# Optimization experiments

Measured on AMD Instinct MI355X. Metric: run time of the kernel, lower is better.

The kernel has to match this reference:

```python
import jax, jax.numpy as jnp
import numpy as np


def _kabsch_rmsd(p, c):
    # p, c: [N, 3]
    pm = jnp.mean(p, axis=0)  # [3]
    cm = jnp.mean(c, axis=0)  # [3]
    # 3x3 cross-covariance
    A = (p - pm).T @ (c - cm)
    U, S, Vt = jnp.linalg.svd(A, full_matrices=False)
    d = jnp.sign(jnp.linalg.det(A))
    # corr_mat = diag([1, 1, d]);  rotation = U @ corr_mat @ Vt
    scale = jnp.concatenate([jnp.ones((2,), dtype=p.dtype), d[None].astype(p.dtype)])
    R = U @ (scale[:, None] * Vt)  # [3,3]
    # translation = pm - R @ cm; aligned coords = (R @ c^T)^T + translation
    aligned = c @ R.T + (pm - R @ cm)
    sq = jnp.sum((p - aligned) ** 2, axis=1)  # [N]
    return jnp.sqrt(jnp.mean(sq))


def setup_inputs() -> dict:
    key = jax.random.key(0)
    k1, k2 = jax.random.split(key)
    B, N = 4096, 2048
    coords_pred = jax.random.normal(k1, (B, N, 3), dtype=jnp.float32)
    coords = jax.random.normal(k2, (B, N, 3), dtype=jnp.float32)
    return {"coords_pred": coords_pred, "coords": coords}


def reference(coords_pred, coords):
    # Batched Kabsch alignment + RMSD; default mode='global', return_all=False
    # -> mean over the per-sample RMSDs.
    rmsds = jax.vmap(_kabsch_rmsd)(coords_pred, coords)  # [B]
    return jnp.mean(rmsds)
```

## Files before the change

### kernel.cpp

```cpp
#include <hip/hip_runtime.h>
#include <math.h>

#define NPTS 2048
#define BLOCK 256

__global__ __launch_bounds__(BLOCK) void kabsch_kernel(
    const float* __restrict__ P, const float* __restrict__ C,
    float* __restrict__ out, int B) {
  const int b = blockIdx.x;
  const int t = threadIdx.x;
  const float4* p4 = (const float4*)(P + (size_t)b * (NPTS * 3));
  const float4* c4 = (const float4*)(C + (size_t)b * (NPTS * 3));

  float acc[17];
#pragma unroll
  for (int i = 0; i < 17; i++) acc[i] = 0.f;

#pragma unroll
  for (int k = 0; k < (NPTS * 3 / 4) / (BLOCK * 3); k++) {
    const int base = k * (BLOCK * 3) + 3 * t;
    const float4 pa = p4[base], pb = p4[base + 1], pq = p4[base + 2];
    const float4 ca = c4[base], cb = c4[base + 1], cq = c4[base + 2];
    const float Px[4] = {pa.x, pa.w, pb.z, pq.y};
    const float Py[4] = {pa.y, pb.x, pb.w, pq.z};
    const float Pz[4] = {pa.z, pb.y, pq.x, pq.w};
    const float Cx[4] = {ca.x, ca.w, cb.z, cq.y};
    const float Cy[4] = {ca.y, cb.x, cb.w, cq.z};
    const float Cz[4] = {ca.z, cb.y, cq.x, cq.w};
#pragma unroll
    for (int i = 0; i < 4; i++) {
      const float px = Px[i], py = Py[i], pz = Pz[i];
      const float cx = Cx[i], cy = Cy[i], cz = Cz[i];
      acc[0] += px; acc[1] += py; acc[2] += pz;
      acc[3] += cx; acc[4] += cy; acc[5] += cz;
      acc[6] += px * px + py * py + pz * pz;
      acc[7] += cx * cx + cy * cy + cz * cz;
      acc[8]  += px * cx; acc[9]  += px * cy; acc[10] += px * cz;
      acc[11] += py * cx; acc[12] += py * cy; acc[13] += py * cz;
      acc[14] += pz * cx; acc[15] += pz * cy; acc[16] += pz * cz;
    }
  }

#pragma unroll
  for (int off = 32; off > 0; off >>= 1) {
#pragma unroll
    for (int i = 0; i < 17; i++) acc[i] += __shfl_down(acc[i], off);
  }
  __shared__ float red[BLOCK / 64][17];
  const int wave = t >> 6, lane = t & 63;
  if (lane == 0) {
#pragma unroll
    for (int i = 0; i < 17; i++) red[wave][i] = acc[i];
  }
  __syncthreads();

  if (t == 0) {
    double s[17];
#pragma unroll
    for (int i = 0; i < 17; i++) {
      float v = red[0][i];
      for (int w = 1; w < BLOCK / 64; w++) v += red[w][i];
      s[i] = (double)v;
    }
    const double invN = 1.0 / (double)NPTS;
    const double spx = s[0], spy = s[1], spz = s[2];
    const double scx = s[3], scy = s[4], scz = s[5];
    const double Ep = s[6] - (spx * spx + spy * spy + spz * spz) * invN;
    const double Ec = s[7] - (scx * scx + scy * scy + scz * scz) * invN;
    const double a00 = s[8]  - spx * scx * invN, a01 = s[9]  - spx * scy * invN, a02 = s[10] - spx * scz * invN;
    const double a10 = s[11] - spy * scx * invN, a11 = s[12] - spy * scy * invN, a12 = s[13] - spy * scz * invN;
    const double a20 = s[14] - spz * scx * invN, a21 = s[15] - spz * scy * invN, a22 = s[16] - spz * scz * invN;
    const double det = a00 * (a11 * a22 - a12 * a21)
                     - a01 * (a10 * a22 - a12 * a20)
                     + a02 * (a10 * a21 - a11 * a20);
    const double b00 = a00 * a00 + a10 * a10 + a20 * a20;
    const double b11 = a01 * a01 + a11 * a11 + a21 * a21;
    const double b22 = a02 * a02 + a12 * a12 + a22 * a22;
    const double b01 = a00 * a01 + a10 * a11 + a20 * a21;
    const double b02 = a00 * a02 + a10 * a12 + a20 * a22;
    const double b12 = a01 * a02 + a11 * a12 + a21 * a22;
    const double q = (b00 + b11 + b22) / 3.0;
    const double p1 = b01 * b01 + b02 * b02 + b12 * b12;
    const double d0 = b00 - q, d1 = b11 - q, d2 = b22 - q;
    const double p2 = d0 * d0 + d1 * d1 + d2 * d2 + 2.0 * p1;
    double e1, e2, e3;
    if (p2 < 1e-30) {
      e1 = e2 = e3 = q;
    } else {
      const double pp = sqrt(p2 / 6.0);
      const double inv = 1.0 / pp;
      const double c00 = d0 * inv, c11 = d1 * inv, c22 = d2 * inv;
      const double c01 = b01 * inv, c02 = b02 * inv, c12 = b12 * inv;
      double r = 0.5 * (c00 * (c11 * c22 - c12 * c12)
                      - c01 * (c01 * c22 - c12 * c02)
                      + c02 * (c01 * c12 - c11 * c02));
      r = fmin(1.0, fmax(-1.0, r));
      const double phi = acos(r) / 3.0;
      e1 = q + 2.0 * pp * cos(phi);
      e3 = q + 2.0 * pp * cos(phi + 2.0943951023931953);
      e2 = 3.0 * q - e1 - e3;
    }
    const double s1 = sqrt(fmax(e1, 0.0));
    const double s2 = sqrt(fmax(e2, 0.0));
    const double s3 = sqrt(fmax(e3, 0.0));
    const double dsign = (det > 0.0) ? 1.0 : ((det < 0.0) ? -1.0 : 0.0);
    const double trRS = s1 + s2 + dsign * s3;
    const double msd = (Ep + Ec - 2.0 * trRS) * invN;
    const double rmsd = sqrt(fmax(msd, 0.0));
    atomicAdd(out, (float)(rmsd / (double)B));
  }
}

extern "C" void kernel_launch(void* const* d_in, const int* in_sizes, int n_in,
                              void* d_out, int out_size, void* d_ws, size_t ws_size,
                              hipStream_t stream) {
  const float* P = (const float*)d_in[0];
  const float* C = (const float*)d_in[1];
  float* out = (float*)d_out;
  const int B = in_sizes[0] / (NPTS * 3);
  hipMemsetAsync(out, 0, sizeof(float), stream);
  kabsch_kernel<<<B, BLOCK, 0, stream>>>(P, C, out, B);
}
```

Before: 218.0 us.

## Assign one wavefront per sample with register prefetch and separate mean reduction

Each wavefront now handles one whole sample, with 4 samples per block, so the LDS reduction, the block barrier and the single-thread serial epilogue are no longer shared across a block. The loop software-prefetches the next chunk of float4 loads into registers to overlap memory latency with the FMAs. Per-sample RMSDs go to a workspace and a second single-block kernel averages them. This replaces the memset and the global float atomics but adds a second launch and higher register pressure.

```diff
diff --git a/kernel.cpp b/kernel.cpp
--- a/kernel.cpp
+++ b/kernel.cpp
@@ -3,12 +3,17 @@
 
 #define NPTS 2048
 #define BLOCK 256
+#define WPB 4
+#define ITERS 8
 
-__global__ __launch_bounds__(BLOCK) void kabsch_kernel(
+__global__ __launch_bounds__(BLOCK, 4) void kabsch_kernel(
     const float* __restrict__ P, const float* __restrict__ C,
-    float* __restrict__ out, int B) {
-  const int b = blockIdx.x;
-  const int t = threadIdx.x;
+    float* __restrict__ rmsd_out, int B) {
+  const int wave = threadIdx.x >> 6;
+  const int lane = threadIdx.x & 63;
+  const int b = blockIdx.x * WPB + wave;
+  if (b >= B) return;
+
   const float4* p4 = (const float4*)(P + (size_t)b * (NPTS * 3));
   const float4* c4 = (const float4*)(C + (size_t)b * (NPTS * 3));
 
@@ -16,11 +21,18 @@
 #pragma unroll
   for (int i = 0; i < 17; i++) acc[i] = 0.f;
 
+  int base = 3 * lane;
+  float4 pa = p4[base], pb = p4[base + 1], pq = p4[base + 2];
+  float4 ca = c4[base], cb = c4[base + 1], cq = c4[base + 2];
+
 #pragma unroll
-  for (int k = 0; k < (NPTS * 3 / 4) / (BLOCK * 3); k++) {
-    const int base = k * (BLOCK * 3) + 3 * t;
-    const float4 pa = p4[base], pb = p4[base + 1], pq = p4[base + 2];
-    const float4 ca = c4[base], cb = c4[base + 1], cq = c4[base + 2];
+  for (int k = 0; k < ITERS; k++) {
+    float4 npa, npb, npq, nca, ncb, ncq;
+    if (k < ITERS - 1) {
+      const int nb_ = base + 192;
+      npa = p4[nb_]; npb = p4[nb_ + 1]; npq = p4[nb_ + 2];
+      nca = c4[nb_]; ncb = c4[nb_ + 1]; ncq = c4[nb_ + 2];
+    }
     const float Px[4] = {pa.x, pa.w, pb.z, pq.y};
     const float Py[4] = {pa.y, pb.x, pb.w, pq.z};
     const float Pz[4] = {pa.z, pb.y, pq.x, pq.w};
@@ -39,6 +51,9 @@
       acc[11] += py * cx; acc[12] += py * cy; acc[13] += py * cz;
       acc[14] += pz * cx; acc[15] += pz * cy; acc[16] += pz * cz;
     }
+    pa = npa; pb = npb; pq = npq;
+    ca = nca; cb = ncb; cq = ncq;
+    base += 192;
   }
 
 #pragma unroll
@@ -46,22 +61,11 @@
 #pragma unroll
     for (int i = 0; i < 17; i++) acc[i] += __shfl_down(acc[i], off);
   }
-  __shared__ float red[BLOCK / 64][17];
-  const int wave = t >> 6, lane = t & 63;
+
   if (lane == 0) {
-#pragma unroll
-    for (int i = 0; i < 17; i++) red[wave][i] = acc[i];
-  }
-  __syncthreads();
-
-  if (t == 0) {
     double s[17];
 #pragma unroll
-    for (int i = 0; i < 17; i++) {
-      float v = red[0][i];
-      for (int w = 1; w < BLOCK / 64; w++) v += red[w][i];
-      s[i] = (double)v;
-    }
+    for (int i = 0; i < 17; i++) s[i] = (double)acc[i];
     const double invN = 1.0 / (double)NPTS;
     const double spx = s[0], spy = s[1], spz = s[2];
     const double scx = s[3], scy = s[4], scz = s[5];
@@ -106,8 +110,24 @@
     const double dsign = (det > 0.0) ? 1.0 : ((det < 0.0) ? -1.0 : 0.0);
     const double trRS = s1 + s2 + dsign * s3;
     const double msd = (Ep + Ec - 2.0 * trRS) * invN;
-    const double rmsd = sqrt(fmax(msd, 0.0));
-    atomicAdd(out, (float)(rmsd / (double)B));
+    rmsd_out[b] = (float)sqrt(fmax(msd, 0.0));
+  }
+}
+
+__global__ __launch_bounds__(BLOCK) void mean_kernel(
+    const float* __restrict__ rmsd, float* __restrict__ out, int B) {
+  float s = 0.f;
+  for (int i = threadIdx.x; i < B; i += BLOCK) s += rmsd[i];
+#pragma unroll
+  for (int off = 32; off > 0; off >>= 1) s += __shfl_down(s, off);
+  __shared__ float sm[BLOCK / 64];
+  const int wave = threadIdx.x >> 6, lane = threadIdx.x & 63;
+  if (lane == 0) sm[wave] = s;
+  __syncthreads();
+  if (threadIdx.x == 0) {
+    float tot = 0.f;
+    for (int w = 0; w < BLOCK / 64; w++) tot += sm[w];
+    out[0] = tot / (float)B;
   }
 }
 
@@ -117,7 +137,9 @@
   const float* P = (const float*)d_in[0];
   const float* C = (const float*)d_in[1];
   float* out = (float*)d_out;
+  float* ws = (float*)d_ws;
   const int B = in_sizes[0] / (NPTS * 3);
-  hipMemsetAsync(out, 0, sizeof(float), stream);
-  kabsch_kernel<<<B, BLOCK, 0, stream>>>(P, C, out, B);
+  const int grid = (B + WPB - 1) / WPB;
+  kabsch_kernel<<<grid, BLOCK, 0, stream>>>(P, C, ws, B);
+  mean_kernel<<<1, BLOCK, 0, stream>>>(ws, out, B);
 }
```

Measured after the change: 223.2 us. 2.4% more time.
